# Kernel optimization log

Measured on AMD Instinct MI355X. Metric: run time of the kernel, lower is better.

Reference implementation:

```python
import jax, jax.numpy as jnp
import numpy as np

H = 64  # rnn_size == input_size
CANVAS = 25


def _init_params(key, vocab_size):
    ks = jax.random.split(key, 14)
    s = 0.05
    p = {}
    p['embed'] = jax.random.normal(ks[0], (vocab_size + 1, H), jnp.float32) * s
    p['W_ih'] = jax.random.normal(ks[1], (4 * H, H), jnp.float32) * s
    p['W_hh'] = jax.random.normal(ks[2], (4 * H, H), jnp.float32) * s
    p['b_ih'] = jax.random.normal(ks[3], (4 * H,), jnp.float32) * s
    p['b_hh'] = jax.random.normal(ks[4], (4 * H,), jnp.float32) * s
    p['Wc'] = jax.random.normal(ks[5], (3, H), jnp.float32) * s
    p['bc'] = jax.random.normal(ks[6], (3,), jnp.float32) * s
    p['Ws'] = jax.random.normal(ks[7], (3, H), jnp.float32) * s
    p['bs'] = jax.random.normal(ks[8], (3,), jnp.float32) * s
    p['Wo'] = jax.random.normal(ks[9], (2, H), jnp.float32) * s
    p['bo'] = jax.random.normal(ks[10], (2,), jnp.float32) * s
    p['Wr1'] = jax.random.normal(ks[11], (32, H + 1 + 4), jnp.float32) * s
    p['br1'] = jnp.zeros((32,), jnp.float32)
    p['Wr2'] = jax.random.normal(ks[12], (1, 32), jnp.float32) * s
    p['br2'] = jnp.zeros((1,), jnp.float32)
    return p


def setup_inputs() -> dict:
    key = jax.random.key(0)
    k1, k2, k3, k4, k5 = jax.random.split(key, 5)
    B, T, V = 4096, 128, 32000
    inp = {
        'inst': jax.random.randint(k1, (B, T), 0, V, dtype=jnp.int64)
        if jax.config.jax_enable_x64 else jax.random.randint(k1, (B, T), 0, V, dtype=jnp.int32),
        'prev_canvas': jax.random.normal(k2, (B, CANVAS, 4), jnp.float32),
        'ref_obj': jax.random.normal(k3, (B, 4), jnp.float32),
        'target_obj': jax.random.normal(k4, (B, 4), jnp.float32),
    }
    inp.update(_init_params(k5, V))
    return inp


def _encode(inst, embed, W_ih, W_hh, b_ih, b_hh):
    # inst: [B, T] -> h: [B, H] via sequential LSTMCell
    xs = embed[inst]                       # [B, T, H]
    xs = jnp.swapaxes(xs, 0, 1)            # [T, B, H]
    B = inst.shape[0]
    h0 = jnp.zeros((B, H), xs.dtype)
    c0 = jnp.zeros((B, H), xs.dtype)

    def step(carry, x):
        h, c = carry
        gates = x @ W_ih.T + b_ih + h @ W_hh.T + b_hh   # [B, 4H]
        i, f, g, o = jnp.split(gates, 4, axis=-1)
        i, f, o = jax.nn.sigmoid(i), jax.nn.sigmoid(f), jax.nn.sigmoid(o)
        c = f * c + i * jnp.tanh(g)
        h = o * jnp.tanh(c)
        return (h, c), None

    (h, _), _ = jax.lax.scan(step, (h0, c0), xs)
    return h


def _act_tag(inst):
    # 1.0 if last token with value >= 1 equals 9, else 0.0
    T = inst.shape[1]
    mask = inst >= 1                                   # [B, T]
    last_pos = T - 1 - jnp.argmax(mask[:, ::-1], axis=1)
    last_val = jnp.take_along_axis(inst, last_pos[:, None], axis=1)[:, 0]
    tag = jnp.where((last_val == 9) & mask.any(axis=1), 1.0, 0.0)
    return tag.astype(jnp.float32)


def reference(inst, prev_canvas, ref_obj, target_obj, embed, W_ih, W_hh, b_ih, b_hh,
              Wc, bc, Ws, bs, Wo, bo, Wr1, br1, Wr2, br2):
    h = _encode(inst, embed, W_ih, W_hh, b_ih, b_hh)           # [B, H]
    tag = _act_tag(inst)                                       # [B]
    inst2 = jnp.concatenate([h, tag[:, None]], axis=1)         # [B, H+1]
    inst2 = jnp.broadcast_to(inst2[:, None, :], (h.shape[0], CANVAS, H + 1))
    feat = jnp.concatenate([inst2, prev_canvas], axis=2)       # [B, 25, 69]
    hid = jax.nn.relu(jnp.einsum('bnf,of->bno', feat, Wr1) + br1)
    score = (jnp.einsum('bno,ro->bnr', hid, Wr2) + br2)[..., 0]  # [B, 25]
    weight = jax.nn.softmax(score, axis=1)
    ref_pred = jnp.einsum('bn,bnd->bd', weight, prev_canvas)   # [B, 4]
    offset = jnp.clip(h @ Wo.T + bo, -1.0, 1.0)                # hardtanh, [B, 2]
    color_out = jax.nn.log_softmax(h @ Wc.T + bc, axis=1)      # [B, 3]
    shape_out = jax.nn.log_softmax(h @ Ws.T + bs, axis=1)      # [B, 3]
    row_out = ref_pred[:, 2] + offset[:, 0]
    col_out = ref_pred[:, 3] + offset[:, 1]
    return (color_out, shape_out, row_out, col_out)
```

## Files before the change

### kernel.cpp

```cpp
#include <hip/hip_runtime.h>
#include <hip/hip_bf16.h>

#define HH 64
#define TT 128
#define BT 8

typedef __attribute__((ext_vector_type(8))) short bf16x8;
typedef __attribute__((ext_vector_type(4))) float f32x4;

__device__ __forceinline__ unsigned short f2bf(float f) {
  union { float f; unsigned u; } v; v.f = f;
  return (unsigned short)((v.u + 0x7FFFu + ((v.u >> 16) & 1u)) >> 16);
}
__device__ __forceinline__ float rcp_(float x) { return __builtin_amdgcn_rcpf(x); }
__device__ __forceinline__ float exp2_(float x) { return __builtin_amdgcn_exp2f(x); }

#define L2E 1.44269504f
#define L2E2 2.88539008f

__device__ __forceinline__ float red32(float v) {
#pragma unroll
  for (int s = 16; s; s >>= 1) v += __shfl_xor(v, s, 32);
  return v;
}

__global__ void convert_embed(const float* __restrict__ src,
                              unsigned short* __restrict__ dst, int n) {
  int base = (blockIdx.x * 256 + threadIdx.x) * 4;
  if (base + 4 <= n) {
    float4 v = *(const float4*)(src + base);
    ushort4 r;
    r.x = f2bf(v.x); r.y = f2bf(v.y); r.z = f2bf(v.z); r.w = f2bf(v.w);
    *(ushort4*)(dst + base) = r;
  } else {
    for (int k = base; k < n; k++) dst[k] = f2bf(src[k]);
  }
}

#define MFMA(acc, a, b) acc = __builtin_amdgcn_mfma_f32_16x16x32_bf16(a, b, acc, 0, 0, 0)

__global__ __launch_bounds__(256, 2) void lstm_k(
    const int* __restrict__ inst, const unsigned short* __restrict__ ebf,
    const float* __restrict__ Wih, const float* __restrict__ Whh,
    const float* __restrict__ bih, const float* __restrict__ bhh,
    const float* __restrict__ canvas,
    const float* __restrict__ Wc, const float* __restrict__ bc,
    const float* __restrict__ Ws, const float* __restrict__ bs,
    const float* __restrict__ Wo, const float* __restrict__ bo,
    const float* __restrict__ Wr1, const float* __restrict__ br1,
    const float* __restrict__ Wr2, const float* __restrict__ br2,
    float* __restrict__ out, int B)
{
  __shared__ int tokT[TT * BT];
  __shared__ unsigned short hsh[2 * BT * HH];
  __shared__ float h_s[BT][HH + 2];
  __shared__ float Wr1_s[32 * 69];
  __shared__ float cv_s[BT * 100];

  const int tid  = threadIdx.x;
  const int lane = tid & 63;
  const int w    = tid >> 6;
  const int fr   = lane & 15;
  const int fg   = lane >> 4;
  const int b0   = blockIdx.x * BT;
  const int jcol = w * 16 + fr;
  const int hi2  = fg >> 1;
  const int row0 = (fg & 1) * 4 + hi2 * 2;

  for (int i = tid; i < BT * TT; i += 256) {
    const int b = i >> 7, t = i & (TT - 1);
    tokT[t * BT + b] = inst[(size_t)(b0 + b) * TT + t];
  }
  for (int i = tid; i < 2 * BT * HH; i += 256) hsh[i] = 0;
  for (int i = tid; i < 32 * 69; i += 256) Wr1_s[i] = Wr1[i];
  for (int i = tid; i < BT * 100; i += 256) cv_s[i] = canvas[(size_t)b0 * 100 + i];

  bf16x8 wt[4][2][2];
#pragma unroll
  for (int q = 0; q < 4; q++) {
    const int n = (w + q * 4) * 16 + fr;
#pragma unroll
    for (int kt = 0; kt < 2; kt++) {
      const float* pa = Wih + n * 64 + kt * 32 + fg * 8;
      const float* pb = Whh + n * 64 + kt * 32 + fg * 8;
      bf16x8 fa, fb;
#pragma unroll
      for (int j = 0; j < 8; j++) { fa[j] = (short)f2bf(pa[j]); fb[j] = (short)f2bf(pb[j]); }
      wt[q][kt][0] = fa; wt[q][kt][1] = fb;
    }
  }
  const float nbi = -L2E  * (bih[jcol]       + bhh[jcol]);
  const float nbf = -L2E  * (bih[64 + jcol]  + bhh[64 + jcol]);
  const float sbg =  L2E2 * (bih[128 + jcol] + bhh[128 + jcol]);
  const float nbo = -L2E  * (bih[192 + jcol] + bhh[192 + jcol]);

  const int rr7 = fr & 7;
  const int ra  = (rr7 * 128 + fg * 16) ^ (rr7 << 4);
  const int rb  = (rr7 * 128 + 64 + fg * 16) ^ (rr7 << 4);
  const int wa0 = (row0 * 128 + 2 * jcol) ^ ((row0 & 7) << 4);
  const int wa1 = ((row0 + 1) * 128 + 2 * jcol) ^ (((row0 + 1) & 7) << 4);
  char* const hs0 = (char*)hsh;
  char* const hs1 = hs0 + BT * HH * 2;

  __syncthreads();

  bf16x8 xa0, xa1;
  {
    const int tk = tokT[0 * BT + rr7];
    const unsigned short* p = ebf + tk * 64 + fg * 8;
    xa0 = *(const bf16x8*)p; xa1 = *(const bf16x8*)(p + 32);
  }
  float cst0 = 0.f, cst1 = 0.f, hk0 = 0.f, hk1 = 0.f;

#define LSTM_STEP(RD, WR, T)                                                   \
  {                                                                            \
    bf16x8 ha0 = *(const bf16x8*)(RD + ra);                                    \
    bf16x8 ha1 = *(const bf16x8*)(RD + rb);                                    \
    const int tn = ((T) + 1 < TT) ? (T) + 1 : TT - 1;                          \
    const int tk = tokT[tn * BT + rr7];                                        \
    const unsigned short* px = ebf + tk * 64 + fg * 8;                         \
    bf16x8 xn0 = *(const bf16x8*)px;                                           \
    bf16x8 xn1 = *(const bf16x8*)(px + 32);                                    \
    f32x4 D0 = {0.f,0.f,0.f,0.f}, D1 = {0.f,0.f,0.f,0.f},                      \
          D2 = {0.f,0.f,0.f,0.f}, D3 = {0.f,0.f,0.f,0.f};                      \
    MFMA(D0, xa0, wt[0][0][0]); MFMA(D0, xa1, wt[0][1][0]);                    \
    MFMA(D1, xa0, wt[1][0][0]); MFMA(D1, xa1, wt[1][1][0]);                    \
    MFMA(D2, xa0, wt[2][0][0]); MFMA(D2, xa1, wt[2][1][0]);                    \
    MFMA(D3, xa0, wt[3][0][0]); MFMA(D3, xa1, wt[3][1][0]);                    \
    MFMA(D0, ha0, wt[0][0][1]); MFMA(D0, ha1, wt[0][1][1]);                    \
    MFMA(D1, ha0, wt[1][0][1]); MFMA(D1, ha1, wt[1][1][1]);                    \
    MFMA(D2, ha0, wt[2][0][1]); MFMA(D2, ha1, wt[2][1][1]);                    \
    MFMA(D3, ha0, wt[3][0][1]); MFMA(D3, ha1, wt[3][1][1]);                    \
    {                                                                          \
      const float i_ = hi2 ? D0[2] : D0[0];                                    \
      const float f_ = hi2 ? D1[2] : D1[0];                                    \
      const float g_ = hi2 ? D2[2] : D2[0];                                    \
      const float o_ = hi2 ? D3[2] : D3[0];                                    \
      const float gi = rcp_(1.f + exp2_(fmaf(i_, -L2E, nbi)));                 \
      const float gf = rcp_(1.f + exp2_(fmaf(f_, -L2E, nbf)));                 \
      const float eg = exp2_(fminf(fmaf(g_, L2E2, sbg), 60.f));                \
      const float tg = (eg - 1.f) * rcp_(eg + 1.f);                            \
      const float go = rcp_(1.f + exp2_(fmaf(o_, -L2E, nbo)));                 \
      const float c  = fmaf(gf, cst0, gi * tg);                                \
      cst0 = c;                                                                \
      const float ec = exp2_(L2E2 * fminf(c, 8.f));                            \
      const float th = (ec - 1.f) * rcp_(ec + 1.f);                            \
      hk0 = go * th;                                                           \
      union { float f; unsigned u; } cv; cv.f = hk0;                           \
      *(unsigned short*)(WR + wa0) = (unsigned short)((cv.u + 0x8000u) >> 16); \
    }                                                                          \
    {                                                                          \
      const float i_ = hi2 ? D0[3] : D0[1];                                    \
      const float f_ = hi2 ? D1[3] : D1[1];                                    \
      const float g_ = hi2 ? D2[3] : D2[1];                                    \
      const float o_ = hi2 ? D3[3] : D3[1];                                    \
      const float gi = rcp_(1.f + exp2_(fmaf(i_, -L2E, nbi)));                 \
      const float gf = rcp_(1.f + exp2_(fmaf(f_, -L2E, nbf)));                 \
      const float eg = exp2_(fminf(fmaf(g_, L2E2, sbg), 60.f));                \
      const float tg = (eg - 1.f) * rcp_(eg + 1.f);                            \
      const float go = rcp_(1.f + exp2_(fmaf(o_, -L2E, nbo)));                 \
      const float c  = fmaf(gf, cst1, gi * tg);                                \
      cst1 = c;                                                                \
      const float ec = exp2_(L2E2 * fminf(c, 8.f));                            \
      const float th = (ec - 1.f) * rcp_(ec + 1.f);                            \
      hk1 = go * th;                                                           \
      union { float f; unsigned u; } cv; cv.f = hk1;                           \
      *(unsigned short*)(WR + wa1) = (unsigned short)((cv.u + 0x8000u) >> 16); \
    }                                                                          \
    __syncthreads();                                                           \
    xa0 = xn0; xa1 = xn1;                                                      \
  }

  for (int t = 0; t < TT; t += 2) {
    LSTM_STEP(hs0, hs1, t);
    LSTM_STEP(hs1, hs0, t + 1);
  }
#undef LSTM_STEP

  h_s[row0][jcol]     = hk0;
  h_s[row0 + 1][jcol] = hk1;
  __syncthreads();

  const int m  = tid >> 5;
  const int o  = tid & 31;
  const int gb = b0 + m;

  int key = -1;
#pragma unroll
  for (int q = 0; q < 4; q++) {
    const int t = o + q * 32;
    const int tk = tokT[t * BT + m];
    if (tk >= 1) key = max(key, (t << 16) | tk);
  }
#pragma unroll
  for (int s = 16; s; s >>= 1) key = max(key, __shfl_xor(key, s, 32));
  const float tag = (key >= 0 && (key & 0xFFFF) == 9) ? 1.f : 0.f;

  float base = br1[o] + Wr1_s[o * 69 + 64] * tag;
  for (int f = 0; f < 64; f++) base += Wr1_s[o * 69 + f] * h_s[m][f];
  const float wr2o = Wr2[o];
  const float* cv = cv_s + m * 100;

  float sc[25];
  float mx = -1e30f;
#pragma unroll
  for (int n = 0; n < 25; n++) {
    float acc = base;
#pragma unroll
    for (int d = 0; d < 4; d++) acc += Wr1_s[o * 69 + 65 + d] * cv[n * 4 + d];
    float p = wr2o * fmaxf(acc, 0.f);
#pragma unroll
    for (int s = 16; s; s >>= 1) p += __shfl_xor(p, s, 32);
    sc[n] = p + br2[0];
    mx = fmaxf(mx, sc[n]);
  }
  float sum = 0.f, rp2 = 0.f, rp3 = 0.f;
#pragma unroll
  for (int n = 0; n < 25; n++) {
    const float e = __expf(sc[n] - mx);
    sum += e;
    rp2 += e * cv[n * 4 + 2];
    rp3 += e * cv[n * 4 + 3];
  }
  const float inv = 1.f / sum;

  const float h0 = h_s[m][o], h1 = h_s[m][o + 32];
  float c0 = red32(h0 * Wc[o]       + h1 * Wc[32 + o])  + bc[0];
  float c1 = red32(h0 * Wc[64 + o]  + h1 * Wc[96 + o])  + bc[1];
  float c2 = red32(h0 * Wc[128 + o] + h1 * Wc[160 + o]) + bc[2];
  float s0 = red32(h0 * Ws[o]       + h1 * Ws[32 + o])  + bs[0];
  float s1 = red32(h0 * Ws[64 + o]  + h1 * Ws[96 + o])  + bs[1];
  float s2 = red32(h0 * Ws[128 + o] + h1 * Ws[160 + o]) + bs[2];
  float o0 = red32(h0 * Wo[o]       + h1 * Wo[32 + o])  + bo[0];
  float o1 = red32(h0 * Wo[64 + o]  + h1 * Wo[96 + o])  + bo[1];
  o0 = fminf(fmaxf(o0, -1.f), 1.f);
  o1 = fminf(fmaxf(o1, -1.f), 1.f);

  const float cm = fmaxf(c0, fmaxf(c1, c2));
  const float cl = cm + __logf(__expf(c0 - cm) + __expf(c1 - cm) + __expf(c2 - cm));
  const float sm = fmaxf(s0, fmaxf(s1, s2));
  const float sl = sm + __logf(__expf(s0 - sm) + __expf(s1 - sm) + __expf(s2 - sm));

  if (o == 0) {
    out[gb * 3 + 0] = c0 - cl; out[gb * 3 + 1] = c1 - cl; out[gb * 3 + 2] = c2 - cl;
    float* shp = out + (size_t)3 * B;
    shp[gb * 3 + 0] = s0 - sl; shp[gb * 3 + 1] = s1 - sl; shp[gb * 3 + 2] = s2 - sl;
    out[(size_t)6 * B + gb] = rp2 * inv + o0;
    out[(size_t)7 * B + gb] = rp3 * inv + o1;
  }
}

extern "C" void kernel_launch(void* const* d_in, const int* in_sizes, int n_in,
                              void* d_out, int out_size, void* d_ws, size_t ws_size,
                              hipStream_t stream) {
  const int*   inst   = (const int*)  d_in[0];
  const float* canvas = (const float*)d_in[1];
  const float* embed  = (const float*)d_in[4];
  const float* Wih    = (const float*)d_in[5];
  const float* Whh    = (const float*)d_in[6];
  const float* bih    = (const float*)d_in[7];
  const float* bhh    = (const float*)d_in[8];
  const float* Wc     = (const float*)d_in[9];
  const float* bc     = (const float*)d_in[10];
  const float* Ws_    = (const float*)d_in[11];
  const float* bs     = (const float*)d_in[12];
  const float* Wo     = (const float*)d_in[13];
  const float* bo     = (const float*)d_in[14];
  const float* Wr1    = (const float*)d_in[15];
  const float* br1    = (const float*)d_in[16];
  const float* Wr2    = (const float*)d_in[17];
  const float* br2    = (const float*)d_in[18];

  const int B  = in_sizes[0] / TT;
  const int NE = in_sizes[4];

  unsigned short* ebf = (unsigned short*)d_ws;

  convert_embed<<<(NE / 4 + 255) / 256, 256, 0, stream>>>(embed, ebf, NE);
  lstm_k<<<B / BT, 256, 0, stream>>>(inst, ebf, Wih, Whh, bih, bhh,
                                     canvas, Wc, bc, Ws_, bs, Wo, bo,
                                     Wr1, br1, Wr2, br2, (float*)d_out, B);
}
```

Before: 107.7 us.

## Fill all 16 MFMA rows per block and simplify LSTM gate math

Doubles the batch tile per block from 8 to 16 sequences, so each 16x16 MFMA tile carries useful rows instead of half of them duplicating the same sequences. Each lane now updates four LSTM cell states per step, and the grid drops to one block per CU. The token table is stored row-major with padding, and the next token's embedding load is moved between the input and recurrent MFMAs. The gate nonlinearities are merged to use fewer reciprocals, at the cost of dropping the clamp on the g-gate exponent, which risks inf/NaN for large inputs. Having only one block per CU also reduces the latency hiding that came from running two blocks concurrently.

```diff
diff --git a/kernel.cpp b/kernel.cpp
--- a/kernel.cpp
+++ b/kernel.cpp
@@ -3,14 +3,15 @@
 
 #define HH 64
 #define TT 128
-#define BT 8
+#define TP 132
+#define BT 16
 
 typedef __attribute__((ext_vector_type(8))) short bf16x8;
 typedef __attribute__((ext_vector_type(4))) float f32x4;
 
 __device__ __forceinline__ unsigned short f2bf(float f) {
   union { float f; unsigned u; } v; v.f = f;
-  return (unsigned short)((v.u + 0x7FFFu + ((v.u >> 16) & 1u)) >> 16);
+  return (unsigned short)((v.u + 0x8000u) >> 16);
 }
 __device__ __forceinline__ float rcp_(float x) { return __builtin_amdgcn_rcpf(x); }
 __device__ __forceinline__ float exp2_(float x) { return __builtin_amdgcn_exp2f(x); }
@@ -39,7 +40,7 @@
 
 #define MFMA(acc, a, b) acc = __builtin_amdgcn_mfma_f32_16x16x32_bf16(a, b, acc, 0, 0, 0)
 
-__global__ __launch_bounds__(256, 2) void lstm_k(
+__global__ __launch_bounds__(256, 1) void lstm_k(
     const int* __restrict__ inst, const unsigned short* __restrict__ ebf,
     const float* __restrict__ Wih, const float* __restrict__ Whh,
     const float* __restrict__ bih, const float* __restrict__ bhh,
@@ -51,9 +52,9 @@
     const float* __restrict__ Wr2, const float* __restrict__ br2,
     float* __restrict__ out, int B)
 {
-  __shared__ int tokT[TT * BT];
+  __shared__ int tokT[BT * TP];
   __shared__ unsigned short hsh[2 * BT * HH];
-  __shared__ float h_s[BT][HH + 2];
+  __shared__ float h_s[BT][68];
   __shared__ float Wr1_s[32 * 69];
   __shared__ float cv_s[BT * 100];
 
@@ -64,14 +65,12 @@
   const int fg   = lane >> 4;
   const int b0   = blockIdx.x * BT;
   const int jcol = w * 16 + fr;
-  const int hi2  = fg >> 1;
-  const int row0 = (fg & 1) * 4 + hi2 * 2;
 
   for (int i = tid; i < BT * TT; i += 256) {
     const int b = i >> 7, t = i & (TT - 1);
-    tokT[t * BT + b] = inst[(size_t)(b0 + b) * TT + t];
-  }
-  for (int i = tid; i < 2 * BT * HH; i += 256) hsh[i] = 0;
+    tokT[b * TP + t] = inst[(size_t)(b0 + b) * TT + t];
+  }
+  for (int i = tid; i < BT * HH; i += 256) hsh[i] = 0;
   for (int i = tid; i < 32 * 69; i += 256) Wr1_s[i] = Wr1[i];
   for (int i = tid; i < BT * 100; i += 256) cv_s[i] = canvas[(size_t)b0 * 100 + i];
 
@@ -85,7 +84,11 @@
       const float* pb = Whh + n * 64 + kt * 32 + fg * 8;
       bf16x8 fa, fb;
 #pragma unroll
-      for (int j = 0; j < 8; j++) { fa[j] = (short)f2bf(pa[j]); fb[j] = (short)f2bf(pb[j]); }
+      for (int j = 0; j < 8; j++) {
+        union { float f; unsigned u; } va, vb; va.f = pa[j]; vb.f = pb[j];
+        fa[j] = (short)((va.u + 0x8000u) >> 16);
+        fb[j] = (short)((vb.u + 0x8000u) >> 16);
+      }
       wt[q][kt][0] = fa; wt[q][kt][1] = fb;
     }
   }
@@ -94,78 +97,62 @@
   const float sbg =  L2E2 * (bih[128 + jcol] + bhh[128 + jcol]);
   const float nbo = -L2E  * (bih[192 + jcol] + bhh[192 + jcol]);
 
-  const int rr7 = fr & 7;
-  const int ra  = (rr7 * 128 + fg * 16) ^ (rr7 << 4);
-  const int rb  = (rr7 * 128 + 64 + fg * 16) ^ (rr7 << 4);
-  const int wa0 = (row0 * 128 + 2 * jcol) ^ ((row0 & 7) << 4);
-  const int wa1 = ((row0 + 1) * 128 + 2 * jcol) ^ (((row0 + 1) & 7) << 4);
+  const int sx = (fr & 7) << 4;
+  const int ra = (fr * 128 + fg * 16) ^ sx;
+  const int rb = (fr * 128 + 64 + fg * 16) ^ sx;
+  int wa[4];
+#pragma unroll
+  for (int r = 0; r < 4; r++) {
+    const int m = fg * 4 + r;
+    wa[r] = (m * 128 + 2 * jcol) ^ ((m & 7) << 4);
+  }
   char* const hs0 = (char*)hsh;
   char* const hs1 = hs0 + BT * HH * 2;
+  const int* const tokrow = tokT + fr * TP;
 
   __syncthreads();
 
   bf16x8 xa0, xa1;
   {
-    const int tk = tokT[0 * BT + rr7];
+    const int tk = tokrow[0];
     const unsigned short* p = ebf + tk * 64 + fg * 8;
     xa0 = *(const bf16x8*)p; xa1 = *(const bf16x8*)(p + 32);
   }
-  float cst0 = 0.f, cst1 = 0.f, hk0 = 0.f, hk1 = 0.f;
+  float cst[4] = {0.f, 0.f, 0.f, 0.f};
+  float hk[4];
+  const f32x4 z4 = {0.f, 0.f, 0.f, 0.f};
 
 #define LSTM_STEP(RD, WR, T)                                                   \
   {                                                                            \
-    bf16x8 ha0 = *(const bf16x8*)(RD + ra);                                    \
-    bf16x8 ha1 = *(const bf16x8*)(RD + rb);                                    \
-    const int tn = ((T) + 1 < TT) ? (T) + 1 : TT - 1;                          \
-    const int tk = tokT[tn * BT + rr7];                                        \
-    const unsigned short* px = ebf + tk * 64 + fg * 8;                         \
-    bf16x8 xn0 = *(const bf16x8*)px;                                           \
-    bf16x8 xn1 = *(const bf16x8*)(px + 32);                                    \
-    f32x4 D0 = {0.f,0.f,0.f,0.f}, D1 = {0.f,0.f,0.f,0.f},                      \
-          D2 = {0.f,0.f,0.f,0.f}, D3 = {0.f,0.f,0.f,0.f};                      \
+    const int tknext = tokrow[((T) + 1) & (TT - 1)];                           \
+    bf16x8 ha0 = *(const bf16x8*)((RD) + ra);                                  \
+    bf16x8 ha1 = *(const bf16x8*)((RD) + rb);                                  \
+    f32x4 D0 = z4, D1 = z4, D2 = z4, D3 = z4;                                  \
     MFMA(D0, xa0, wt[0][0][0]); MFMA(D0, xa1, wt[0][1][0]);                    \
     MFMA(D1, xa0, wt[1][0][0]); MFMA(D1, xa1, wt[1][1][0]);                    \
     MFMA(D2, xa0, wt[2][0][0]); MFMA(D2, xa1, wt[2][1][0]);                    \
     MFMA(D3, xa0, wt[3][0][0]); MFMA(D3, xa1, wt[3][1][0]);                    \
+    const unsigned short* px = ebf + tknext * 64 + fg * 8;                     \
+    bf16x8 xn0 = *(const bf16x8*)px;                                           \
+    bf16x8 xn1 = *(const bf16x8*)(px + 32);                                    \
     MFMA(D0, ha0, wt[0][0][1]); MFMA(D0, ha1, wt[0][1][1]);                    \
     MFMA(D1, ha0, wt[1][0][1]); MFMA(D1, ha1, wt[1][1][1]);                    \
     MFMA(D2, ha0, wt[2][0][1]); MFMA(D2, ha1, wt[2][1][1]);                    \
     MFMA(D3, ha0, wt[3][0][1]); MFMA(D3, ha1, wt[3][1][1]);                    \
-    {                                                                          \
-      const float i_ = hi2 ? D0[2] : D0[0];                                    \
-      const float f_ = hi2 ? D1[2] : D1[0];                                    \
-      const float g_ = hi2 ? D2[2] : D2[0];                                    \
-      const float o_ = hi2 ? D3[2] : D3[0];                                    \
-      const float gi = rcp_(1.f + exp2_(fmaf(i_, -L2E, nbi)));                 \
-      const float gf = rcp_(1.f + exp2_(fmaf(f_, -L2E, nbf)));                 \
-      const float eg = exp2_(fminf(fmaf(g_, L2E2, sbg), 60.f));                \
-      const float tg = (eg - 1.f) * rcp_(eg + 1.f);                            \
-      const float go = rcp_(1.f + exp2_(fmaf(o_, -L2E, nbo)));                 \
-      const float c  = fmaf(gf, cst0, gi * tg);                                \
-      cst0 = c;                                                                \
-      const float ec = exp2_(L2E2 * fminf(c, 8.f));                            \
-      const float th = (ec - 1.f) * rcp_(ec + 1.f);                            \
-      hk0 = go * th;                                                           \
-      union { float f; unsigned u; } cv; cv.f = hk0;                           \
-      *(unsigned short*)(WR + wa0) = (unsigned short)((cv.u + 0x8000u) >> 16); \
-    }                                                                          \
-    {                                                                          \
-      const float i_ = hi2 ? D0[3] : D0[1];                                    \
-      const float f_ = hi2 ? D1[3] : D1[1];                                    \
-      const float g_ = hi2 ? D2[3] : D2[1];                                    \
-      const float o_ = hi2 ? D3[3] : D3[1];                                    \
-      const float gi = rcp_(1.f + exp2_(fmaf(i_, -L2E, nbi)));                 \
-      const float gf = rcp_(1.f + exp2_(fmaf(f_, -L2E, nbf)));                 \
-      const float eg = exp2_(fminf(fmaf(g_, L2E2, sbg), 60.f));                \
-      const float tg = (eg - 1.f) * rcp_(eg + 1.f);                            \
-      const float go = rcp_(1.f + exp2_(fmaf(o_, -L2E, nbo)));                 \
-      const float c  = fmaf(gf, cst1, gi * tg);                                \
-      cst1 = c;                                                                \
-      const float ec = exp2_(L2E2 * fminf(c, 8.f));                            \
-      const float th = (ec - 1.f) * rcp_(ec + 1.f);                            \
-      hk1 = go * th;                                                           \
-      union { float f; unsigned u; } cv; cv.f = hk1;                           \
-      *(unsigned short*)(WR + wa1) = (unsigned short)((cv.u + 0x8000u) >> 16); \
+    _Pragma("unroll")                                                          \
+    for (int r = 0; r < 4; r++) {                                              \
+      const float pi = exp2_(fmaf(D0[r], -L2E, nbi));               \
+      const float pf = exp2_(fmaf(D1[r], -L2E, nbf));               \
+      const float eg = exp2_(fmaf(D2[r], L2E2, sbg));               \
+      const float po = exp2_(fmaf(D3[r], -L2E, nbo));               \
+      const float a  = (eg - 1.f) * rcp_((1.f + pi) * (eg + 1.f));             \
+      const float c  = fmaf(rcp_(1.f + pf), cst[r], a);                        \
+      cst[r] = c;                                                              \
+      const float ec = exp2_(fminf(L2E2 * c, 60.f));                \
+      const float hn = (ec - 1.f) * rcp_((1.f + po) * (ec + 1.f));             \
+      hk[r] = hn;                                                              \
+      union { float f; unsigned u; } cv; cv.f = hn;                            \
+      *(unsigned short*)((WR) + wa[r]) = (unsigned short)((cv.u + 0x8000u) >> 16); \
     }                                                                          \
     __syncthreads();                                                           \
     xa0 = xn0; xa1 = xn1;                                                      \
@@ -177,76 +164,78 @@
   }
 #undef LSTM_STEP
 
-  h_s[row0][jcol]     = hk0;
-  h_s[row0 + 1][jcol] = hk1;
+#pragma unroll
+  for (int r = 0; r < 4; r++) h_s[fg * 4 + r][jcol] = hk[r];
   __syncthreads();
 
-  const int m  = tid >> 5;
-  const int o  = tid & 31;
-  const int gb = b0 + m;
-
-  int key = -1;
-#pragma unroll
-  for (int q = 0; q < 4; q++) {
-    const int t = o + q * 32;
-    const int tk = tokT[t * BT + m];
-    if (tk >= 1) key = max(key, (t << 16) | tk);
-  }
-#pragma unroll
-  for (int s = 16; s; s >>= 1) key = max(key, __shfl_xor(key, s, 32));
-  const float tag = (key >= 0 && (key & 0xFFFF) == 9) ? 1.f : 0.f;
-
-  float base = br1[o] + Wr1_s[o * 69 + 64] * tag;
-  for (int f = 0; f < 64; f++) base += Wr1_s[o * 69 + f] * h_s[m][f];
-  const float wr2o = Wr2[o];
-  const float* cv = cv_s + m * 100;
-
-  float sc[25];
-  float mx = -1e30f;
-#pragma unroll
-  for (int n = 0; n < 25; n++) {
-    float acc = base;
-#pragma unroll
-    for (int d = 0; d < 4; d++) acc += Wr1_s[o * 69 + 65 + d] * cv[n * 4 + d];
-    float p = wr2o * fmaxf(acc, 0.f);
-#pragma unroll
-    for (int s = 16; s; s >>= 1) p += __shfl_xor(p, s, 32);
-    sc[n] = p + br2[0];
-    mx = fmaxf(mx, sc[n]);
-  }
-  float sum = 0.f, rp2 = 0.f, rp3 = 0.f;
-#pragma unroll
-  for (int n = 0; n < 25; n++) {
-    const float e = __expf(sc[n] - mx);
-    sum += e;
-    rp2 += e * cv[n * 4 + 2];
-    rp3 += e * cv[n * 4 + 3];
-  }
-  const float inv = 1.f / sum;
-
-  const float h0 = h_s[m][o], h1 = h_s[m][o + 32];
-  float c0 = red32(h0 * Wc[o]       + h1 * Wc[32 + o])  + bc[0];
-  float c1 = red32(h0 * Wc[64 + o]  + h1 * Wc[96 + o])  + bc[1];
-  float c2 = red32(h0 * Wc[128 + o] + h1 * Wc[160 + o]) + bc[2];
-  float s0 = red32(h0 * Ws[o]       + h1 * Ws[32 + o])  + bs[0];
-  float s1 = red32(h0 * Ws[64 + o]  + h1 * Ws[96 + o])  + bs[1];
-  float s2 = red32(h0 * Ws[128 + o] + h1 * Ws[160 + o]) + bs[2];
-  float o0 = red32(h0 * Wo[o]       + h1 * Wo[32 + o])  + bo[0];
-  float o1 = red32(h0 * Wo[64 + o]  + h1 * Wo[96 + o])  + bo[1];
-  o0 = fminf(fmaxf(o0, -1.f), 1.f);
-  o1 = fminf(fmaxf(o1, -1.f), 1.f);
-
-  const float cm = fmaxf(c0, fmaxf(c1, c2));
-  const float cl = cm + __logf(__expf(c0 - cm) + __expf(c1 - cm) + __expf(c2 - cm));
-  const float sm = fmaxf(s0, fmaxf(s1, s2));
-  const float sl = sm + __logf(__expf(s0 - sm) + __expf(s1 - sm) + __expf(s2 - sm));
-
-  if (o == 0) {
-    out[gb * 3 + 0] = c0 - cl; out[gb * 3 + 1] = c1 - cl; out[gb * 3 + 2] = c2 - cl;
-    float* shp = out + (size_t)3 * B;
-    shp[gb * 3 + 0] = s0 - sl; shp[gb * 3 + 1] = s1 - sl; shp[gb * 3 + 2] = s2 - sl;
-    out[(size_t)6 * B + gb] = rp2 * inv + o0;
-    out[(size_t)7 * B + gb] = rp3 * inv + o1;
+  for (int p = 0; p < 2; p++) {
+    const int m  = p * 8 + (tid >> 5);
+    const int o  = tid & 31;
+    const int gb = b0 + m;
+
+    int key = -1;
+#pragma unroll
+    for (int q = 0; q < 4; q++) {
+      const int t = o + q * 32;
+      const int tk = tokT[m * TP + t];
+      if (tk >= 1) key = max(key, (t << 16) | tk);
+    }
+#pragma unroll
+    for (int s = 16; s; s >>= 1) key = max(key, __shfl_xor(key, s, 32));
+    const float tag = (key >= 0 && (key & 0xFFFF) == 9) ? 1.f : 0.f;
+
+    float base = br1[o] + Wr1_s[o * 69 + 64] * tag;
+    for (int f = 0; f < 64; f++) base += Wr1_s[o * 69 + f] * h_s[m][f];
+    const float wr2o = Wr2[o];
+    const float* cv = cv_s + m * 100;
+
+    float sc[25];
+    float mx = -1e30f;
+#pragma unroll
+    for (int n = 0; n < 25; n++) {
+      float acc = base;
+#pragma unroll
+      for (int d = 0; d < 4; d++) acc += Wr1_s[o * 69 + 65 + d] * cv[n * 4 + d];
+      float pp = wr2o * fmaxf(acc, 0.f);
+#pragma unroll
+      for (int s = 16; s; s >>= 1) pp += __shfl_xor(pp, s, 32);
+      sc[n] = pp + br2[0];
+      mx = fmaxf(mx, sc[n]);
+    }
+    float sum = 0.f, rp2 = 0.f, rp3 = 0.f;
+#pragma unroll
+    for (int n = 0; n < 25; n++) {
+      const float e = __expf(sc[n] - mx);
+      sum += e;
+      rp2 += e * cv[n * 4 + 2];
+      rp3 += e * cv[n * 4 + 3];
+    }
+    const float inv = 1.f / sum;
+
+    const float h0 = h_s[m][o], h1 = h_s[m][o + 32];
+    float c0 = red32(h0 * Wc[o]       + h1 * Wc[32 + o])  + bc[0];
+    float c1 = red32(h0 * Wc[64 + o]  + h1 * Wc[96 + o])  + bc[1];
+    float c2 = red32(h0 * Wc[128 + o] + h1 * Wc[160 + o]) + bc[2];
+    float s0 = red32(h0 * Ws[o]       + h1 * Ws[32 + o])  + bs[0];
+    float s1 = red32(h0 * Ws[64 + o]  + h1 * Ws[96 + o])  + bs[1];
+    float s2 = red32(h0 * Ws[128 + o] + h1 * Ws[160 + o]) + bs[2];
+    float o0 = red32(h0 * Wo[o]       + h1 * Wo[32 + o])  + bo[0];
+    float o1 = red32(h0 * Wo[64 + o]  + h1 * Wo[96 + o])  + bo[1];
+    o0 = fminf(fmaxf(o0, -1.f), 1.f);
+    o1 = fminf(fmaxf(o1, -1.f), 1.f);
+
+    const float cm = fmaxf(c0, fmaxf(c1, c2));
+    const float cl = cm + __logf(__expf(c0 - cm) + __expf(c1 - cm) + __expf(c2 - cm));
+    const float sm = fmaxf(s0, fmaxf(s1, s2));
+    const float sl = sm + __logf(__expf(s0 - sm) + __expf(s1 - sm) + __expf(s2 - sm));
+
+    if (o == 0) {
+      out[gb * 3 + 0] = c0 - cl; out[gb * 3 + 1] = c1 - cl; out[gb * 3 + 2] = c2 - cl;
+      float* shp = out + (size_t)3 * B;
+      shp[gb * 3 + 0] = s0 - sl; shp[gb * 3 + 1] = s1 - sl; shp[gb * 3 + 2] = s2 - sl;
+      out[(size_t)6 * B + gb] = rp2 * inv + o0;
+      out[(size_t)7 * B + gb] = rp3 * inv + o1;
+    }
   }
 }
 
```

Result: faster. 98.66 us (-8.4%).
